# Kernel tuning notes

Measured on AMD Instinct MI355X. Metric: run time of the kernel, lower is better.

The kernel has to match this reference:

```python
import jax, jax.numpy as jnp
import numpy as np
import math

HIDDEN = 1024
NUM_HEADS = 16
NUM_GROUPS = 16  # source einsum/rearrange only shape-checks when groups == heads
HEAD_DIM = HIDDEN // NUM_HEADS


def rope(x, base=10000.0):
    # x: [b, s, d]; applied to the FULL hidden vector before head split, as in source.
    # Source rope_fn has a reshape bug; this is the intended rotate-half RoPE with
    # half_d frequencies 1/base^(i/half_d) (== 1/base^(2i/d)).
    b, s, d = x.shape
    half = d // 2
    x1, x2 = x[..., :half], x[..., half:]
    pos = jnp.arange(s, dtype=x.dtype)[:, None]                          # [s,1]
    inv_freq = 1.0 / (base ** (jnp.arange(half, dtype=x.dtype) / half))  # [half]
    ang = pos * inv_freq[None, :]                                        # [s,half]
    sin = jnp.sin(ang)[None]                                             # [1,s,half]
    cos = jnp.cos(ang)[None]
    return jnp.concatenate([x1 * cos - x2 * sin, x2 * cos + x1 * sin], axis=-1)


def setup_inputs() -> dict:
    key = jax.random.key(0)
    ks = jax.random.split(key, 10)
    scale = 1.0 / math.sqrt(HIDDEN)
    inp = {
        "x": jax.random.normal(ks[0], (2, 2048, HIDDEN), dtype=jnp.float32),
        "attn_mask": jax.random.randint(ks[1], (2, 2048), 0, 2, dtype=jnp.int32),
        "Wq": jax.random.uniform(ks[2], (HIDDEN, HIDDEN), jnp.float32, -scale, scale),
        "bq": jax.random.uniform(ks[3], (HIDDEN,), jnp.float32, -scale, scale),
        "Wk": jax.random.uniform(ks[4], (HIDDEN, HIDDEN), jnp.float32, -scale, scale),
        "bk": jax.random.uniform(ks[5], (HIDDEN,), jnp.float32, -scale, scale),
        "Wv": jax.random.uniform(ks[6], (HIDDEN, HIDDEN), jnp.float32, -scale, scale),
        "bv": jax.random.uniform(ks[7], (HIDDEN,), jnp.float32, -scale, scale),
        "Wo": jax.random.uniform(ks[8], (HIDDEN, HIDDEN), jnp.float32, -scale, scale),
        "bo": jax.random.uniform(ks[9], (HIDDEN,), jnp.float32, -scale, scale),
    }
    return inp


def reference(x, attn_mask, Wq, bq, Wk, bk, Wv, bv, Wo, bo):
    b, s, _ = x.shape
    g = NUM_GROUPS
    subh = NUM_HEADS // g  # = 1 here
    d = HIDDEN // g        # per-group dim (== head dim when g == h)

    q = rope(x @ Wq.T + bq)
    k = rope(x @ Wk.T + bk)
    v = x @ Wv.T + bv

    # q: b s (g subh d) -> b g subh s d ; k,v: b s (g d) -> b g s d
    q = q.reshape(b, s, g, subh, d).transpose(0, 2, 3, 1, 4)
    k = k.reshape(b, s, g, d).transpose(0, 2, 1, 3)
    v = v.reshape(b, s, g, d).transpose(0, 2, 1, 3)

    e = jnp.einsum('bghqd,bgkd->bghqk', q, k) / math.sqrt(HEAD_DIM)  # [b,g,subh,s,s]
    mask5 = attn_mask[:, None, None, None, :]  # broadcast over g, subh, query
    e = jnp.where(mask5 == 0, -jnp.inf, e)
    attn = jax.nn.softmax(e, axis=-1)
    out = jnp.einsum('bghqk,bgkd->bghqd', attn, v)            # [b,g,subh,s,d]
    out = out.transpose(0, 3, 1, 2, 4).reshape(b, s, HIDDEN)  # b s (g subh d)
    return out @ Wo.T + bo
```

## Files before the change

### kernel.cpp

```cpp
#include <hip/hip_runtime.h>
#include <hip/hip_bf16.h>


constexpr int Bb  = 2;
constexpr int Ss  = 2048;
constexpr int Hh  = 1024;
constexpr int NHh = 16;
constexpr int Mm  = Bb * Ss;

typedef __attribute__((ext_vector_type(8))) unsigned short ushort8;
typedef __attribute__((ext_vector_type(8))) short short8;
typedef __attribute__((ext_vector_type(4))) float f32x4;
typedef __attribute__((ext_vector_type(4))) unsigned int u32x4;

__device__ __forceinline__ unsigned short f2bf(float f) {
    unsigned int u = __float_as_uint(f);
    u += 0x7fffu + ((u >> 16) & 1u);
    return (unsigned short)(u >> 16);
}
__device__ __forceinline__ float bf2f(unsigned short h) {
    return __uint_as_float(((unsigned int)h) << 16);
}
__device__ __forceinline__ void gload16(const void* g, void* l) {
    __builtin_amdgcn_global_load_lds(
        (const __attribute__((address_space(1))) unsigned int*)g,
        (__attribute__((address_space(3))) unsigned int*)l, 16, 0, 0);
}

__global__ __launch_bounds__(256) void convert_k(
    const float* __restrict__ x,
    const float* __restrict__ Wq, const float* __restrict__ Wk,
    const float* __restrict__ Wv, const float* __restrict__ Wo,
    unsigned short* __restrict__ xb, unsigned short* __restrict__ wall)
{
    size_t e = ((size_t)blockIdx.x * 256 + threadIdx.x) << 3;
    const float* s; unsigned short* d;
    if (e < (size_t)Mm * Hh) {
        s = x + e; d = xb + e;
    } else {
        size_t f = e - (size_t)Mm * Hh;
        int t = (int)(f >> 20);
        const float* w = (t == 0) ? Wq : (t == 1) ? Wk : (t == 2) ? Wv : Wo;
        s = w + (f & 1048575);
        d = wall + f;
    }
    float4 a = *(const float4*)s;
    float4 b = *(const float4*)(s + 4);
    ushort8 o;
    o[0] = f2bf(a.x); o[1] = f2bf(a.y); o[2] = f2bf(a.z); o[3] = f2bf(a.w);
    o[4] = f2bf(b.x); o[5] = f2bf(b.y); o[6] = f2bf(b.z); o[7] = f2bf(b.w);
    *(ushort8*)d = o;
}

#define GEMM_BODY(ATYPE_PTR, WPTR, K0MAX)                                          \
    __shared__ unsigned short As[128 * 64];                                        \
    __shared__ unsigned short Bs[128 * 64];                                        \
    const int tid  = threadIdx.x;                                                  \
    const int lane = tid & 63;                                                     \
    const int w    = tid >> 6;                                                     \
    const int wr   = w >> 1, wc = w & 1;                                           \
    const int l16  = lane & 15, g = lane >> 4;                                     \
    const int R0   = blockIdx.x * 128;                                             \
    char* asb = (char*)As; char* bsb = (char*)Bs;                                  \
    f32x4 acc[4][4] = {};                                                          \
    for (int k0 = 0; k0 < K0MAX; k0 += 64) {                                       \
        _Pragma("unroll")                                                          \
        for (int it = 0; it < 4; ++it) {                                           \
            int sbase = w * 4096 + it * 1024;                                      \
            int boff  = sbase + lane * 16;                                         \
            int r     = boff >> 7;                                                 \
            int c     = (boff >> 4) & 7;                                           \
            int col   = k0 + ((c ^ (r & 7)) << 3);                                 \
            gload16(&ATYPE_PTR[(size_t)(R0 + r) * 1024 + col], asb + sbase);       \
            gload16(&WPTR[(size_t)(gn + r) * 1024 + col], bsb + sbase);            \
        }                                                                          \
        __syncthreads();                                                           \
        short8 bfrag[4][2];                                                        \
        _Pragma("unroll")                                                          \
        for (int u = 0; u < 4; ++u) {                                              \
            int row = wc * 64 + u * 16 + l16;                                      \
            _Pragma("unroll")                                                      \
            for (int s = 0; s < 2; ++s)                                            \
                bfrag[u][s] = *(const short8*)(bsb + row * 128 +                   \
                               ((s * 64 + g * 16) ^ ((row & 7) << 4)));            \
        }                                                                          \
        _Pragma("unroll")                                                          \
        for (int t = 0; t < 4; ++t) {                                              \
            int row = wr * 64 + t * 16 + l16;                                      \
            short8 af[2];                                                          \
            _Pragma("unroll")                                                      \
            for (int s = 0; s < 2; ++s)                                            \
                af[s] = *(const short8*)(asb + row * 128 +                         \
                         ((s * 64 + g * 16) ^ ((row & 7) << 4)));                  \
            _Pragma("unroll")                                                      \
            for (int u = 0; u < 4; ++u) {                                          \
                acc[t][u] = __builtin_amdgcn_mfma_f32_16x16x32_bf16(af[0], bfrag[u][0], acc[t][u], 0, 0, 0); \
                acc[t][u] = __builtin_amdgcn_mfma_f32_16x16x32_bf16(af[1], bfrag[u][1], acc[t][u], 0, 0, 0); \
            }                                                                      \
        }                                                                          \
        __syncthreads();                                                           \
    }

__global__ __launch_bounds__(256) void gemm_qkv_k(
    const unsigned short* __restrict__ xb, const unsigned short* __restrict__ wall,
    const float* __restrict__ bq, const float* __restrict__ bk, const float* __restrict__ bv,
    unsigned short* __restrict__ q, unsigned short* __restrict__ k2,
    unsigned short* __restrict__ v)
{
    const int gn = blockIdx.y * 128;
    GEMM_BODY(xb, wall, 1024)

    const int sel = gn >> 10;
    const int n0  = gn & 1023;
    const float* bias = (sel == 0) ? bq : (sel == 1) ? bk : bv;
    unsigned short* outp = (sel == 0) ? q : (sel == 1) ? k2 : v;
    const float qs = (sel == 0) ? 0.18033688011112042f : 1.0f;
    #pragma unroll
    for (int u = 0; u < 4; ++u) {
        int coll = wc * 64 + u * 16 + l16;
        float bb = bias[n0 + coll];
        #pragma unroll
        for (int t = 0; t < 4; ++t)
            #pragma unroll
            for (int rr = 0; rr < 4; ++rr) {
                int row = R0 + wr * 64 + t * 16 + g * 4 + rr;
                outp[(size_t)row * 1024 + n0 + coll] = f2bf((acc[t][u][rr] + bb) * qs);
            }
    }
}

__global__ __launch_bounds__(256) void gemm_out_k(
    const unsigned short* __restrict__ ao, const unsigned short* __restrict__ wo,
    const float* __restrict__ bo, float* __restrict__ out)
{
    const int gn = blockIdx.y * 128;
    GEMM_BODY(ao, wo, 1024)

    #pragma unroll
    for (int u = 0; u < 4; ++u) {
        int coll = wc * 64 + u * 16 + l16;
        float bb = bo[gn + coll];
        #pragma unroll
        for (int t = 0; t < 4; ++t)
            #pragma unroll
            for (int rr = 0; rr < 4; ++rr) {
                int row = R0 + wr * 64 + t * 16 + g * 4 + rr;
                out[(size_t)row * 1024 + gn + coll] = acc[t][u][rr] + bb;
            }
    }
}

__global__ __launch_bounds__(256) void rope_frag_k(
    const unsigned short* __restrict__ qin, const unsigned short* __restrict__ kin,
    unsigned short* __restrict__ qfrag, unsigned short* __restrict__ kfrag)
{
    __shared__ unsigned short Ld[2][64][72];
    const int kt = blockIdx.x;
    const int hp = blockIdx.y;
    const int zz = blockIdx.z;
    const int bz = zz & 1, sel = zz >> 1;
    const unsigned short* src = sel ? kin : qin;
    unsigned short* dstf = sel ? kfrag : qfrag;

    const int t   = threadIdx.x;
    const int r   = t & 63;
    const int c16 = (t >> 6) << 4;
    const int pos = kt * 64 + r;
    const size_t rowb = (size_t)(bz * Ss + pos) * 1024;

    ushort8 A0 = *(const ushort8*)&src[rowb + hp * 64 + c16];
    ushort8 A1 = *(const ushort8*)&src[rowb + hp * 64 + c16 + 8];
    ushort8 B0 = *(const ushort8*)&src[rowb + (hp + 8) * 64 + c16];
    ushort8 B1 = *(const ushort8*)&src[rowb + (hp + 8) * 64 + c16 + 8];

    #pragma unroll
    for (int i = 0; i < 16; ++i) {
        int d = c16 + i;
        float jj  = (float)(hp * 64 + d);
        float inv = exp2f(jj * -0.0259525632621414f);
        float ang = (float)pos * inv;
        float sn, cs;
        __sincosf(ang, &sn, &cs);
        unsigned short ua = (i < 8) ? A0[i] : A1[i - 8];
        unsigned short ub = (i < 8) ? B0[i] : B1[i - 8];
        float a = bf2f(ua), b = bf2f(ub);
        Ld[0][r][d] = f2bf(a * cs - b * sn);
        Ld[1][r][d] = f2bf(b * cs + a * sn);
    }
    __syncthreads();

    #pragma unroll
    for (int cc = 0; cc < 4; ++cc) {
        int c    = t * 4 + cc;
        int hh   = c >> 9;
        int ci   = c & 511;
        int blk  = ci >> 7, s2 = (ci >> 6) & 1, lane2 = ci & 63;
        int gg = lane2 >> 4, ll = lane2 & 15;
        ushort8 o = *(const ushort8*)&Ld[hh][blk * 16 + ll][s2 * 32 + gg * 8];
        size_t base = (size_t)(bz * 16 + hp + hh * 8) * 131072 + (size_t)kt * 4096;
        *(ushort8*)&dstf[base + (size_t)ci * 8] = o;
    }
}

__global__ __launch_bounds__(256) void fragify_v_k(
    const unsigned short* __restrict__ v, unsigned short* __restrict__ vfrag)
{
    __shared__ unsigned short Ld[64][72];
    const int kt = blockIdx.x, bh = blockIdx.y;
    const int bz = bh >> 4, h = bh & 15;
    const int t = threadIdx.x;
    const int r = t & 63, c0 = (t >> 6) << 4;
    const unsigned short* srcp = &v[(size_t)(bz * Ss + kt * 64 + r) * 1024 + h * 64 + c0];
    *(ushort8*)&Ld[r][c0]     = *(const ushort8*)srcp;
    *(ushort8*)&Ld[r][c0 + 8] = *(const ushort8*)(srcp + 8);
    __syncthreads();

    #pragma unroll
    for (int cc = 0; cc < 2; ++cc) {
        int c = t * 2 + cc;
        int dt4 = c >> 7, ks = (c >> 6) & 1, lane2 = c & 63;
        int gg = lane2 >> 4, ll = lane2 & 15;
        ushort8 o;
        #pragma unroll
        for (int e = 0; e < 8; ++e)
            o[e] = Ld[ks * 32 + gg * 8 + e][dt4 * 16 + ll];
        *(ushort8*)&vfrag[(size_t)bh * 131072 + (size_t)kt * 4096 + (size_t)c * 8] = o;
    }
}

#define FLASH_ITER(KC, KN, KT)                                                     \
    {                                                                              \
        const int ktn = ((KT) + 1) & 31;                                           \
        _Pragma("unroll")                                                          \
        for (int i = 0; i < 8; ++i)                                                \
            KN[i] = *(const short8*)&kfb[(size_t)ktn * 4096 + i * 512 + lane * 8]; \
        _Pragma("unroll")                                                          \
        for (int i = 0; i < 8; ++i)                                                \
            VV[i] = *(const short8*)&vfb[(size_t)(KT) * 4096 + i * 512 + lane * 8];\
        int mk[4][4];                                                              \
        _Pragma("unroll")                                                          \
        for (int k4 = 0; k4 < 4; ++k4)                                             \
            *(int4*)&mk[k4][0] =                                                   \
                *(const int4*)&mask[bz * Ss + (KT) * 64 + k4 * 16 + g * 4];        \
        f32x4 S[2][4];                                                             \
        _Pragma("unroll")                                                          \
        for (int t = 0; t < 2; ++t)                                                \
            _Pragma("unroll")                                                      \
            for (int k4 = 0; k4 < 4; ++k4) S[t][k4] = (f32x4)0.f;                  \
        _Pragma("unroll")                                                          \
        for (int k4 = 0; k4 < 4; ++k4)                                             \
            _Pragma("unroll")                                                      \
            for (int t = 0; t < 2; ++t) {                                          \
                S[t][k4] = __builtin_amdgcn_mfma_f32_16x16x32_bf16(                \
                    KC[k4 * 2 + 0], qf[t][0], S[t][k4], 0, 0, 0);                  \
                S[t][k4] = __builtin_amdgcn_mfma_f32_16x16x32_bf16(                \
                    KC[k4 * 2 + 1], qf[t][1], S[t][k4], 0, 0, 0);                  \
            }                                                                      \
        _Pragma("unroll")                                                          \
        for (int t = 0; t < 2; ++t)                                                \
            _Pragma("unroll")                                                      \
            for (int k4 = 0; k4 < 4; ++k4)                                         \
                _Pragma("unroll")                                                  \
                for (int r = 0; r < 4; ++r)                                        \
                    S[t][k4][r] = mk[k4][r] ? S[t][k4][r] : -1e30f;                \
        float rm[2];                                                               \
        _Pragma("unroll")                                                          \
        for (int t = 0; t < 2; ++t) {                                              \
            float m0 = fmaxf(fmaxf(S[t][0][0], S[t][0][1]), fmaxf(S[t][0][2], S[t][0][3])); \
            float m1 = fmaxf(fmaxf(S[t][1][0], S[t][1][1]), fmaxf(S[t][1][2], S[t][1][3])); \
            float m2 = fmaxf(fmaxf(S[t][2][0], S[t][2][1]), fmaxf(S[t][2][2], S[t][2][3])); \
            float m3 = fmaxf(fmaxf(S[t][3][0], S[t][3][1]), fmaxf(S[t][3][2], S[t][3][3])); \
            float m  = fmaxf(fmaxf(m0, m1), fmaxf(m2, m3));                        \
            m = fmaxf(m, __shfl_xor(m, 16));                                       \
            m = fmaxf(m, __shfl_xor(m, 32));                                       \
            rm[t] = m;                                                             \
        }                                                                          \
        bool grow = (rm[0] > mrow[0] + 10.0f) || (rm[1] > mrow[1] + 10.0f);        \
        if (__any((int)grow)) {                                                    \
            float mn0 = fmaxf(mrow[0], rm[0]);                                     \
            float mn1 = fmaxf(mrow[1], rm[1]);                                     \
            float rs0 = exp2f(mrow[0] - mn0);                                      \
            float rs1 = exp2f(mrow[1] - mn1);                                      \
            mrow[0] = mn0; mrow[1] = mn1;                                          \
            _Pragma("unroll")                                                      \
            for (int r = 0; r < 4; ++r) {                                          \
                float f0 = __shfl(rs0, g * 4 + r);                                 \
                float f1 = __shfl(rs1, g * 4 + r);                                 \
                _Pragma("unroll")                                                  \
                for (int dt = 0; dt < 4; ++dt) { O[0][dt][r] *= f0; O[1][dt][r] *= f1; } \
                Osum[0][r] *= f0; Osum[1][r] *= f1;                                \
            }                                                                      \
        }                                                                          \
        _Pragma("unroll")                                                          \
        for (int t = 0; t < 2; ++t) {                                              \
            unsigned int U[4][2];                                                  \
            _Pragma("unroll")                                                      \
            for (int k4 = 0; k4 < 4; ++k4) {                                       \
                float p0 = exp2f(S[t][k4][0] - mrow[t]);                           \
                float p1 = exp2f(S[t][k4][1] - mrow[t]);                           \
                float p2 = exp2f(S[t][k4][2] - mrow[t]);                           \
                float p3 = exp2f(S[t][k4][3] - mrow[t]);                           \
                asm("v_cvt_pk_bf16_f32 %0, %1, %2" : "=v"(U[k4][0]) : "v"(p0), "v"(p1)); \
                asm("v_cvt_pk_bf16_f32 %0, %1, %2" : "=v"(U[k4][1]) : "v"(p2), "v"(p3)); \
            }                                                                      \
                \
            asm("v_permlane32_swap_b32 %0, %1" : "+v"(U[0][0]), "+v"(U[1][0]));    \
            asm("v_permlane32_swap_b32 %0, %1" : "+v"(U[0][1]), "+v"(U[1][1]));    \
            asm("v_permlane32_swap_b32 %0, %1" : "+v"(U[2][0]), "+v"(U[3][0]));    \
            asm("v_permlane32_swap_b32 %0, %1" : "+v"(U[2][1]), "+v"(U[3][1]));    \
            asm("v_permlane16_swap_b32 %0, %1" : "+v"(U[0][0]), "+v"(U[1][0]));    \
            asm("v_permlane16_swap_b32 %0, %1" : "+v"(U[0][1]), "+v"(U[1][1]));    \
            asm("v_permlane16_swap_b32 %0, %1" : "+v"(U[2][0]), "+v"(U[3][0]));    \
            asm("v_permlane16_swap_b32 %0, %1" : "+v"(U[2][1]), "+v"(U[3][1]));    \
            _Pragma("unroll")                                                      \
            for (int ks = 0; ks < 2; ++ks) {                                       \
                u32x4 gp;                                                          \
                gp[0] = U[2 * ks][0]; gp[1] = U[2 * ks][1];                        \
                gp[2] = U[2 * ks + 1][0]; gp[3] = U[2 * ks + 1][1];                \
                short8 pf = __builtin_bit_cast(short8, gp);                        \
                Osum[t] = __builtin_amdgcn_mfma_f32_16x16x32_bf16(pf, ones, Osum[t], 0, 0, 0); \
                _Pragma("unroll")                                                  \
                for (int dt = 0; dt < 4; ++dt)                                     \
                    O[t][dt] = __builtin_amdgcn_mfma_f32_16x16x32_bf16(            \
                        pf, VV[dt * 2 + ks], O[t][dt], 0, 0, 0);                   \
            }                                                                      \
        }                                                                          \
    }

__global__ __launch_bounds__(256, 2) void flash_k(
    const unsigned short* __restrict__ qfrag, const unsigned short* __restrict__ kfrag,
    const unsigned short* __restrict__ vfrag, const int* __restrict__ mask,
    unsigned short* __restrict__ ao)
{
    const int F   = blockIdx.x;
    const int xcd = F & 7, j = F >> 3;
    const int grp = xcd * 4 + (j >> 4);
    const int qb  = j & 15;
    const int h   = grp & 15;
    const int bz  = grp >> 4;

    const int tid  = threadIdx.x;
    const int lane = tid & 63;
    const int w    = tid >> 6;
    const int l16  = lane & 15;
    const int g    = lane >> 4;

    const size_t fb = (size_t)(bz * 16 + h) * 131072;
    const unsigned short* kfb = kfrag + fb;
    const unsigned short* vfb = vfrag + fb;
    const unsigned short* qfb = qfrag + fb;

    const int qrowbase = bz * Ss + qb * 128 + w * 32;

    short8 qf[2][2];
    #pragma unroll
    for (int t = 0; t < 2; ++t)
        #pragma unroll
        for (int s = 0; s < 2; ++s)
            qf[t][s] = *(const short8*)&qfb[(size_t)(qb * 8 + w * 2 + t) * 1024
                                            + s * 512 + lane * 8];

    f32x4 O[2][4];
    #pragma unroll
    for (int t = 0; t < 2; ++t)
        #pragma unroll
        for (int d = 0; d < 4; ++d) O[t][d] = (f32x4)0.f;
    f32x4 Osum[2];
    Osum[0] = (f32x4)0.f; Osum[1] = (f32x4)0.f;
    float mrow[2] = {-1.0e4f, -1.0e4f};

    short8 ones;
    #pragma unroll
    for (int e = 0; e < 8; ++e) ones[e] = (short)0x3F80;

    short8 KA[8], KB[8], VV[8];
    #pragma unroll
    for (int i = 0; i < 8; ++i)
        KA[i] = *(const short8*)&kfb[(size_t)i * 512 + lane * 8];

    for (int kt = 0; kt < 32; kt += 2) {
        FLASH_ITER(KA, KB, kt)
        FLASH_ITER(KB, KA, kt + 1)
    }

    #pragma unroll
    for (int t = 0; t < 2; ++t)
        #pragma unroll
        for (int r = 0; r < 4; ++r) {
            float inv = 1.0f / Osum[t][r];
            int row = qrowbase + t * 16 + g * 4 + r;
            #pragma unroll
            for (int dt = 0; dt < 4; ++dt)
                ao[(size_t)row * 1024 + h * 64 + dt * 16 + l16] = f2bf(O[t][dt][r] * inv);
        }
}

extern "C" void kernel_launch(void* const* d_in, const int* in_sizes, int n_in,
                              void* d_out, int out_size, void* d_ws, size_t ws_size,
                              hipStream_t stream)
{
    const float* x  = (const float*)d_in[0];
    const int*   am = (const int*)d_in[1];
    const float* Wq = (const float*)d_in[2];
    const float* bq = (const float*)d_in[3];
    const float* Wk = (const float*)d_in[4];
    const float* bk = (const float*)d_in[5];
    const float* Wv = (const float*)d_in[6];
    const float* bv = (const float*)d_in[7];
    const float* Wo = (const float*)d_in[8];
    const float* bo = (const float*)d_in[9];
    float* out = (float*)d_out;

    const size_t NE = (size_t)Mm * Hh;
    unsigned short* q     = (unsigned short*)d_ws;
    unsigned short* k     = q + NE;
    unsigned short* v     = k + NE;
    unsigned short* ao    = v + NE;
    unsigned short* xb    = ao + NE;
    unsigned short* wall  = xb + NE;
    unsigned short* wo    = wall + 3u * 1048576u;
    unsigned short* kfrag = wall + 4u * 1048576u;
    unsigned short* qfrag = xb;
    unsigned short* vfrag = q;

    convert_k<<<(2 * NE) / (256 * 8), 256, 0, stream>>>(x, Wq, Wk, Wv, Wo, xb, wall);
    gemm_qkv_k<<<dim3(Mm / 128, 3072 / 128), 256, 0, stream>>>(
        xb, wall, bq, bk, bv, q, k, v);
    rope_frag_k<<<dim3(32, 8, 4), 256, 0, stream>>>(q, k, qfrag, kfrag);
    fragify_v_k<<<dim3(32, 32), 256, 0, stream>>>(v, vfrag);
    flash_k<<<dim3(512), 256, 0, stream>>>(qfrag, kfrag, vfrag, am, ao);
    gemm_out_k<<<dim3(Mm / 128, Hh / 128), 256, 0, stream>>>(ao, wo, bo, out);
}
```

Baseline: 166.5 us.

## Split flash attention over two key halves with combine kernel and MFMA priority

```diff
diff --git a/kernel.cpp b/kernel.cpp
--- a/kernel.cpp
+++ b/kernel.cpp
@@ -230,7 +230,7 @@
 
 #define FLASH_ITER(KC, KN, KT)                                                     \
     {                                                                              \
-        const int ktn = ((KT) + 1) & 31;                                           \
+        const int ktn = kt0 + ((((KT) - kt0) + 1) & 15);                           \
         _Pragma("unroll")                                                          \
         for (int i = 0; i < 8; ++i)                                                \
             KN[i] = *(const short8*)&kfb[(size_t)ktn * 4096 + i * 512 + lane * 8]; \
@@ -247,6 +247,7 @@
         for (int t = 0; t < 2; ++t)                                                \
             _Pragma("unroll")                                                      \
             for (int k4 = 0; k4 < 4; ++k4) S[t][k4] = (f32x4)0.f;                  \
+        __builtin_amdgcn_s_setprio(1);                                             \
         _Pragma("unroll")                                                          \
         for (int k4 = 0; k4 < 4; ++k4)                                             \
             _Pragma("unroll")                                                      \
@@ -256,6 +257,7 @@
                 S[t][k4] = __builtin_amdgcn_mfma_f32_16x16x32_bf16(                \
                     KC[k4 * 2 + 1], qf[t][1], S[t][k4], 0, 0, 0);                  \
             }                                                                      \
+        __builtin_amdgcn_s_setprio(0);                                             \
         _Pragma("unroll")                                                          \
         for (int t = 0; t < 2; ++t)                                                \
             _Pragma("unroll")                                                      \
@@ -303,7 +305,6 @@
                 asm("v_cvt_pk_bf16_f32 %0, %1, %2" : "=v"(U[k4][0]) : "v"(p0), "v"(p1)); \
                 asm("v_cvt_pk_bf16_f32 %0, %1, %2" : "=v"(U[k4][1]) : "v"(p2), "v"(p3)); \
             }                                                                      \
-                \
             asm("v_permlane32_swap_b32 %0, %1" : "+v"(U[0][0]), "+v"(U[1][0]));    \
             asm("v_permlane32_swap_b32 %0, %1" : "+v"(U[0][1]), "+v"(U[1][1]));    \
             asm("v_permlane32_swap_b32 %0, %1" : "+v"(U[2][0]), "+v"(U[3][0]));    \
@@ -312,6 +313,7 @@
             asm("v_permlane16_swap_b32 %0, %1" : "+v"(U[0][1]), "+v"(U[1][1]));    \
             asm("v_permlane16_swap_b32 %0, %1" : "+v"(U[2][0]), "+v"(U[3][0]));    \
             asm("v_permlane16_swap_b32 %0, %1" : "+v"(U[2][1]), "+v"(U[3][1]));    \
+            __builtin_amdgcn_s_setprio(1);                                         \
             _Pragma("unroll")                                                      \
             for (int ks = 0; ks < 2; ++ks) {                                       \
                 u32x4 gp;                                                          \
@@ -324,20 +326,24 @@
                     O[t][dt] = __builtin_amdgcn_mfma_f32_16x16x32_bf16(            \
                         pf, VV[dt * 2 + ks], O[t][dt], 0, 0, 0);                   \
             }                                                                      \
-        }                                                                          \
-    }
-
-__global__ __launch_bounds__(256, 2) void flash_k(
+            __builtin_amdgcn_s_setprio(0);                                         \
+        }                                                                          \
+    }
+
+__global__ __launch_bounds__(256, 4) void flash_k(
     const unsigned short* __restrict__ qfrag, const unsigned short* __restrict__ kfrag,
     const unsigned short* __restrict__ vfrag, const int* __restrict__ mask,
-    unsigned short* __restrict__ ao)
+    unsigned short* __restrict__ opart, float2* __restrict__ ml)
 {
     const int F   = blockIdx.x;
     const int xcd = F & 7, j = F >> 3;
-    const int grp = xcd * 4 + (j >> 4);
-    const int qb  = j & 15;
+    const int grp = xcd * 4 + (j >> 5);
+    const int rem = j & 31;
+    const int qb  = rem >> 1;
+    const int half = rem & 1;
     const int h   = grp & 15;
     const int bz  = grp >> 4;
+    const int kt0 = half * 16;
 
     const int tid  = threadIdx.x;
     const int lane = tid & 63;
@@ -350,8 +356,6 @@
     const unsigned short* vfb = vfrag + fb;
     const unsigned short* qfb = qfrag + fb;
 
-    const int qrowbase = bz * Ss + qb * 128 + w * 32;
-
     short8 qf[2][2];
     #pragma unroll
     for (int t = 0; t < 2; ++t)
@@ -376,23 +380,59 @@
     short8 KA[8], KB[8], VV[8];
     #pragma unroll
     for (int i = 0; i < 8; ++i)
-        KA[i] = *(const short8*)&kfb[(size_t)i * 512 + lane * 8];
-
-    for (int kt = 0; kt < 32; kt += 2) {
-        FLASH_ITER(KA, KB, kt)
-        FLASH_ITER(KB, KA, kt + 1)
-    }
-
+        KA[i] = *(const short8*)&kfb[(size_t)kt0 * 4096 + i * 512 + lane * 8];
+
+    for (int kt2 = 0; kt2 < 16; kt2 += 2) {
+        FLASH_ITER(KA, KB, kt0 + kt2)
+        FLASH_ITER(KB, KA, kt0 + kt2 + 1)
+    }
+
+    const size_t NE = (size_t)Mm * Hh;
     #pragma unroll
     for (int t = 0; t < 2; ++t)
         #pragma unroll
         for (int r = 0; r < 4; ++r) {
-            float inv = 1.0f / Osum[t][r];
-            int row = qrowbase + t * 16 + g * 4 + r;
+            float osum = Osum[t][r];
+            float inv  = osum > 0.f ? 1.0f / osum : 0.f;
+            float mo   = __shfl(mrow[t], g * 4 + r);
+            int rowl   = qb * 128 + w * 32 + t * 16 + g * 4 + r;
+            size_t ob  = (size_t)half * NE
+                       + ((size_t)(bz * Ss + rowl)) * 1024 + h * 64;
             #pragma unroll
             for (int dt = 0; dt < 4; ++dt)
-                ao[(size_t)row * 1024 + h * 64 + dt * 16 + l16] = f2bf(O[t][dt][r] * inv);
+                opart[ob + dt * 16 + l16] = f2bf(O[t][dt][r] * inv);
+            if (l16 == 0)
+                ml[((half * 2 + bz) * 16 + h) * 2048 + rowl] = make_float2(mo, osum);
         }
+}
+
+__global__ __launch_bounds__(256) void combine_k(
+    const unsigned short* __restrict__ opart, const float2* __restrict__ ml,
+    unsigned short* __restrict__ ao)
+{
+    const size_t NE = (size_t)Mm * Hh;
+    int c    = blockIdx.x * 256 + threadIdx.x;
+    int row  = c >> 7;
+    int col8 = c & 127;
+    int h    = col8 >> 3;
+    int bz   = row >> 11, qrow = row & 2047;
+
+    float2 a = ml[((0 * 2 + bz) * 16 + h) * 2048 + qrow];
+    float2 b = ml[((1 * 2 + bz) * 16 + h) * 2048 + qrow];
+    float M  = fmaxf(a.x, b.x);
+    float w1 = exp2f(a.x - M) * a.y;
+    float w2 = exp2f(b.x - M) * b.y;
+    float tot = w1 + w2;
+    float inv = tot > 0.f ? 1.0f / tot : 0.f;
+    w1 *= inv; w2 *= inv;
+
+    ushort8 o1 = *(const ushort8*)&opart[(size_t)c * 8];
+    ushort8 o2 = *(const ushort8*)&opart[NE + (size_t)c * 8];
+    ushort8 o;
+    #pragma unroll
+    for (int jj = 0; jj < 8; ++jj)
+        o[jj] = f2bf(bf2f(o1[jj]) * w1 + bf2f(o2[jj]) * w2);
+    *(ushort8*)&ao[(size_t)c * 8] = o;
 }
 
 extern "C" void kernel_launch(void* const* d_in, const int* in_sizes, int n_in,
@@ -422,12 +462,15 @@
     unsigned short* kfrag = wall + 4u * 1048576u;
     unsigned short* qfrag = xb;
     unsigned short* vfrag = q;
+    unsigned short* opart = k;
+    float2*         ml    = (float2*)(kfrag + 4u * 1048576u);
 
     convert_k<<<(2 * NE) / (256 * 8), 256, 0, stream>>>(x, Wq, Wk, Wv, Wo, xb, wall);
     gemm_qkv_k<<<dim3(Mm / 128, 3072 / 128), 256, 0, stream>>>(
         xb, wall, bq, bk, bv, q, k, v);
     rope_frag_k<<<dim3(32, 8, 4), 256, 0, stream>>>(q, k, qfrag, kfrag);
     fragify_v_k<<<dim3(32, 32), 256, 0, stream>>>(v, vfrag);
-    flash_k<<<dim3(512), 256, 0, stream>>>(qfrag, kfrag, vfrag, am, ao);
+    flash_k<<<dim3(1024), 256, 0, stream>>>(qfrag, kfrag, vfrag, am, opart, ml);
+    combine_k<<<dim3((Mm * 128) / 256), 256, 0, stream>>>(opart, ml, ao);
     gemm_out_k<<<dim3(Mm / 128, Hh / 128), 256, 0, stream>>>(ao, wo, bo, out);
 }
```

Result: slower. 484.1 us (+190.7%).
